# Kernel tuning notes

Measured on AMD Instinct MI355X. Metric: run time of the kernel, lower is better.

## Reference

```python
import jax, jax.numpy as jnp
import numpy as np

TEMPERATURE = 8.0  # sqrt(d_k=64)

def setup_inputs() -> dict:
    key = jax.random.key(0)
    kq, kk, kv = jax.random.split(key, 3)
    B, S, D = 32, 2048, 64  # B = batch*heads
    q = jax.random.normal(kq, (B, S, D), dtype=jnp.float32)
    k = jax.random.normal(kk, (B, S, D), dtype=jnp.float32)
    v = jax.random.normal(kv, (B, S, D), dtype=jnp.float32)
    return {"q": q, "k": k, "v": v}

def reference(q, k, v):
    # attn = softmax((q @ k^T) / temperature) along key dim; dropout = identity (eval)
    attn = jnp.einsum('bqd,bkd->bqk', q, k) / TEMPERATURE  # [B, S, S]
    attn = jax.nn.softmax(attn, axis=2)
    out = jnp.einsum('bqk,bkd->bqd', attn, v)              # [B, S, D]
    return out
```

## Files before the change

### kernel.cpp

```cpp
#include <hip/hip_runtime.h>
#include <stdint.h>


#define BATCH 32
#define SEQ   2048
#define DIM   64
#define QBLK_WAVE 32
#define NWAVES 4
#define QBLK  (QBLK_WAVE*NWAVES)
#define KVBLK 64
#define NT    (SEQ/KVBLK)

typedef __attribute__((ext_vector_type(8)))  __bf16   bf16x8;
typedef __attribute__((ext_vector_type(16))) float    f32x16;
typedef __attribute__((ext_vector_type(2)))  unsigned uint2v;
typedef __attribute__((ext_vector_type(4)))  unsigned uint4v;

static __device__ __forceinline__ unsigned cvt_pk(float lo, float hi) {
    unsigned r; asm("v_cvt_pk_bf16_f32 %0, %1, %2" : "=v"(r) : "v"(lo), "v"(hi)); return r;
}
static __device__ __forceinline__ float exp2v(float x) {
    float r; asm("v_exp_f32 %0, %1" : "=v"(r) : "v"(x)); return r;
}
static __device__ __forceinline__ float other_half(float v, int hi) {
    unsigned u = __builtin_bit_cast(unsigned, v);
    uint2v r = __builtin_amdgcn_permlane32_swap(u, u, false, false);
    return __builtin_bit_cast(float, hi ? r[0] : r[1]);
}

#define MFMA32(A, B, C) __builtin_amdgcn_mfma_f32_32x32x16_bf16((A), (B), (C), 0, 0, 0)
#define TRR(dst, OFFSTR) \
    asm volatile("ds_read_b64_tr_b16 %0, %1 offset:" OFFSTR : "=v"(dst) : "v"(trbase))

static __device__ __forceinline__ bf16x8 frag_of(uint2v r0, uint2v r1) {
    uint4v w = { r0[0], r0[1], r1[0], r1[1] };
    return __builtin_bit_cast(bf16x8, w);
}

__global__ __launch_bounds__(256, 2)
void attn_fwd_kernel(const float* __restrict__ q,
                     const float* __restrict__ k,
                     const float* __restrict__ v,
                     float* __restrict__ out)
{
    __shared__ unsigned short Ksh[KVBLK * DIM];
    __shared__ unsigned short Vsh[KVBLK * DIM];

    const int id    = blockIdx.x;
    const int swz   = (id & 7) * ((SEQ / QBLK) * BATCH / 8) + (id >> 3);
    const int batch = swz >> 4;
    const int qtile = swz & 15;

    const int t    = threadIdx.x;
    const int lane = t & 63;
    const int wid  = t >> 6;
    const int hi   = lane >> 5;
    const int l31  = lane & 31;
    const int l7   = lane & 7;

    const size_t bbase = (size_t)batch * SEQ * DIM;
    const int q0w = qtile * QBLK + wid * QBLK_WAVE;

    bf16x8 qf[4];
    {
        const float sc = 0.125f * 1.44269504088896341f;
        const float* qp = q + bbase + (size_t)(q0w + l31) * DIM + hi * 8;
        #pragma unroll
        for (int dblk = 0; dblk < 4; ++dblk) {
            float4 f0 = *(const float4*)(qp + dblk * 16);
            float4 f1 = *(const float4*)(qp + dblk * 16 + 4);
            uint4v w = { cvt_pk(f0.x * sc, f0.y * sc), cvt_pk(f0.z * sc, f0.w * sc),
                         cvt_pk(f1.x * sc, f1.y * sc), cvt_pk(f1.z * sc, f1.w * sc) };
            qf[dblk] = __builtin_bit_cast(bf16x8, w);
        }
    }

    const int srow = t >> 2, sq = t & 3;
    const float* kg = k + bbase + (size_t)srow * DIM + sq * 16;
    const float* vg = v + bbase + (size_t)srow * DIM + sq * 16;
    const int ch0 = ((2 * sq)     ^ (srow & 7)) * 8;
    const int ch1 = ((2 * sq + 1) ^ (srow & 7)) * 8;
    unsigned short* ksta = &Ksh[srow * DIM];
    unsigned short* vsta = &Vsh[srow * DIM];

    const int bq = (l31 & 15) >> 2, ee = (lane >> 4) & 1, cc = lane & 3;
    const unsigned vb = (unsigned)(uintptr_t)Vsh;
    const unsigned trbase = vb + (unsigned)((8 * hi + bq) * 128 +
                                            (((2 * ee + (cc >> 1)) ^ bq) * 16) + (cc & 1) * 8);

    const unsigned short* krow = &Ksh[l31 * DIM];

    f32x16 oacc0, oacc1;
    #pragma unroll
    for (int r = 0; r < 16; ++r) { oacc0[r] = 0.f; oacc1[r] = 0.f; }
    float m_run = -3.0e38f, l_run = 0.0f;

    float4 rk[4], rv[4];
    #pragma unroll
    for (int i = 0; i < 4; ++i) {
        rk[i] = *(const float4*)(kg + i * 4);
        rv[i] = *(const float4*)(vg + i * 4);
    }

    #pragma unroll 1
    for (int tile = 0; tile < NT; ++tile) {
        __syncthreads();

        {
            uint4v kw0 = { cvt_pk(rk[0].x, rk[0].y), cvt_pk(rk[0].z, rk[0].w),
                           cvt_pk(rk[1].x, rk[1].y), cvt_pk(rk[1].z, rk[1].w) };
            uint4v kw1 = { cvt_pk(rk[2].x, rk[2].y), cvt_pk(rk[2].z, rk[2].w),
                           cvt_pk(rk[3].x, rk[3].y), cvt_pk(rk[3].z, rk[3].w) };
            uint4v vw0 = { cvt_pk(rv[0].x, rv[0].y), cvt_pk(rv[0].z, rv[0].w),
                           cvt_pk(rv[1].x, rv[1].y), cvt_pk(rv[1].z, rv[1].w) };
            uint4v vw1 = { cvt_pk(rv[2].x, rv[2].y), cvt_pk(rv[2].z, rv[2].w),
                           cvt_pk(rv[3].x, rv[3].y), cvt_pk(rv[3].z, rv[3].w) };
            *(uint4v*)&ksta[ch0] = kw0;
            *(uint4v*)&ksta[ch1] = kw1;
            *(uint4v*)&vsta[ch0] = vw0;
            *(uint4v*)&vsta[ch1] = vw1;
        }
        if (tile + 1 < NT) {
            const float* kg2 = kg + (size_t)(tile + 1) * KVBLK * DIM;
            const float* vg2 = vg + (size_t)(tile + 1) * KVBLK * DIM;
            #pragma unroll
            for (int i = 0; i < 4; ++i) {
                rk[i] = *(const float4*)(kg2 + i * 4);
                rv[i] = *(const float4*)(vg2 + i * 4);
            }
        }
        __syncthreads();

        f32x16 s0, s1;
        #pragma unroll
        for (int r = 0; r < 16; ++r) { s0[r] = 0.f; s1[r] = 0.f; }
        #pragma unroll
        for (int dblk = 0; dblk < 4; ++dblk) {
            int cofs = (((2 * dblk + hi) ^ l7) * 8);
            bf16x8 kf0 = *(const bf16x8*)&krow[cofs];
            bf16x8 kf1 = *(const bf16x8*)&krow[32 * DIM + cofs];
            s0 = MFMA32(kf0, qf[dblk], s0);
            s1 = MFMA32(kf1, qf[dblk], s1);
        }

        uint2v m0k0r0, m0k0r1, m0k1r0, m0k1r1, m0k2r0, m0k2r1, m0k3r0, m0k3r1;
        uint2v m1k0r0, m1k0r1, m1k1r0, m1k1r1, m1k2r0, m1k2r1, m1k3r0, m1k3r1;
        TRR(m0k0r0, "0");    TRR(m0k0r1, "576");
        TRR(m0k1r0, "2048"); TRR(m0k1r1, "2624");
        TRR(m0k2r0, "4096"); TRR(m0k2r1, "4672");
        TRR(m0k3r0, "6144"); TRR(m0k3r1, "6720");
        TRR(m1k0r0, "64");   TRR(m1k0r1, "512");
        TRR(m1k1r0, "2112"); TRR(m1k1r1, "2560");
        TRR(m1k2r0, "4160"); TRR(m1k2r1, "4608");
        TRR(m1k3r0, "6208"); TRR(m1k3r1, "6656");

        float tm = s0[0];
        #pragma unroll
        for (int r = 1; r < 16; ++r) tm = fmaxf(tm, s0[r]);
        #pragma unroll
        for (int r = 0; r < 16; ++r) tm = fmaxf(tm, s1[r]);
        tm = fmaxf(tm, other_half(tm, hi));
        float mn    = fmaxf(m_run, tm);
        float alpha = exp2v(m_run - mn);
        m_run = mn;
        float rs = 0.f;
        #pragma unroll
        for (int r = 0; r < 16; ++r) { s0[r] = exp2v(s0[r] - mn); rs += s0[r]; }
        #pragma unroll
        for (int r = 0; r < 16; ++r) { s1[r] = exp2v(s1[r] - mn); rs += s1[r]; }
        rs += other_half(rs, hi);
        l_run = l_run * alpha + rs;
        #pragma unroll
        for (int r = 0; r < 16; ++r) { oacc0[r] *= alpha; oacc1[r] *= alpha; }

        bf16x8 bfr0, bfr1, bfr2, bfr3;
        {
            uint2v x1 = __builtin_amdgcn_permlane32_swap(cvt_pk(s0[0], s0[1]),  cvt_pk(s0[4], s0[5]),  false, false);
            uint2v x2 = __builtin_amdgcn_permlane32_swap(cvt_pk(s0[2], s0[3]),  cvt_pk(s0[6], s0[7]),  false, false);
            uint4v w = { x1[0], x2[0], x1[1], x2[1] };
            bfr0 = __builtin_bit_cast(bf16x8, w);
            uint2v y1 = __builtin_amdgcn_permlane32_swap(cvt_pk(s0[8], s0[9]),  cvt_pk(s0[12], s0[13]), false, false);
            uint2v y2 = __builtin_amdgcn_permlane32_swap(cvt_pk(s0[10], s0[11]), cvt_pk(s0[14], s0[15]), false, false);
            uint4v w2 = { y1[0], y2[0], y1[1], y2[1] };
            bfr1 = __builtin_bit_cast(bf16x8, w2);
            uint2v z1 = __builtin_amdgcn_permlane32_swap(cvt_pk(s1[0], s1[1]),  cvt_pk(s1[4], s1[5]),  false, false);
            uint2v z2 = __builtin_amdgcn_permlane32_swap(cvt_pk(s1[2], s1[3]),  cvt_pk(s1[6], s1[7]),  false, false);
            uint4v w3 = { z1[0], z2[0], z1[1], z2[1] };
            bfr2 = __builtin_bit_cast(bf16x8, w3);
            uint2v u1 = __builtin_amdgcn_permlane32_swap(cvt_pk(s1[8], s1[9]),  cvt_pk(s1[12], s1[13]), false, false);
            uint2v u2 = __builtin_amdgcn_permlane32_swap(cvt_pk(s1[10], s1[11]), cvt_pk(s1[14], s1[15]), false, false);
            uint4v w4 = { u1[0], u2[0], u1[1], u2[1] };
            bfr3 = __builtin_bit_cast(bf16x8, w4);
        }

        asm volatile("s_waitcnt lgkmcnt(0)" ::: "memory");
        __builtin_amdgcn_sched_barrier(0);

        oacc0 = MFMA32(frag_of(m0k0r0, m0k0r1), bfr0, oacc0);
        oacc1 = MFMA32(frag_of(m1k0r0, m1k0r1), bfr0, oacc1);
        oacc0 = MFMA32(frag_of(m0k1r0, m0k1r1), bfr1, oacc0);
        oacc1 = MFMA32(frag_of(m1k1r0, m1k1r1), bfr1, oacc1);
        oacc0 = MFMA32(frag_of(m0k2r0, m0k2r1), bfr2, oacc0);
        oacc1 = MFMA32(frag_of(m1k2r0, m1k2r1), bfr2, oacc1);
        oacc0 = MFMA32(frag_of(m0k3r0, m0k3r1), bfr3, oacc0);
        oacc1 = MFMA32(frag_of(m1k3r0, m1k3r1), bfr3, oacc1);
    }

    float invl = 1.0f / l_run;
    float* op = out + bbase + (size_t)(q0w + l31) * DIM + 4 * hi;
    #pragma unroll
    for (int rq = 0; rq < 4; ++rq) {
        float4 o0 = { oacc0[4 * rq] * invl, oacc0[4 * rq + 1] * invl,
                      oacc0[4 * rq + 2] * invl, oacc0[4 * rq + 3] * invl };
        float4 o1 = { oacc1[4 * rq] * invl, oacc1[4 * rq + 1] * invl,
                      oacc1[4 * rq + 2] * invl, oacc1[4 * rq + 3] * invl };
        *(float4*)(op + 8 * rq)      = o0;
        *(float4*)(op + 32 + 8 * rq) = o1;
    }
}

extern "C" void kernel_launch(void* const* d_in, const int* in_sizes, int n_in,
                              void* d_out, int out_size, void* d_ws, size_t ws_size,
                              hipStream_t stream) {
    const float* q = (const float*)d_in[0];
    const float* k = (const float*)d_in[1];
    const float* v = (const float*)d_in[2];
    float* out = (float*)d_out;
    dim3 grid((SEQ / QBLK) * BATCH);
    dim3 block(256);
    hipLaunchKernelGGL(attn_fwd_kernel, grid, block, 0, stream, q, k, v, out);
}
```

Measured before the change: 137.5 us.

## Double-buffer K/V in LDS, lazy softmax rescale, tree reductions, MFMA priority

Splits K/V shared memory into two buffers so the next tile is converted and stored while the current one is consumed, leaving one barrier per iteration instead of two. The online softmax now rescales the accumulators only when the row max rises by more than a threshold, skipping most exp and multiply work. Max and sum reductions become trees for more ILP, and s_setprio raises priority around MFMA blocks. The tradeoff is twice the LDS footprint, which may limit occupancy, plus less numerical headroom from the deferred rescaling.

```diff
diff --git a/kernel.cpp b/kernel.cpp
--- a/kernel.cpp
+++ b/kernel.cpp
@@ -10,6 +10,7 @@
 #define QBLK  (QBLK_WAVE*NWAVES)
 #define KVBLK 64
 #define NT    (SEQ/KVBLK)
+#define BUFSHORTS (KVBLK*DIM)
 
 typedef __attribute__((ext_vector_type(8)))  __bf16   bf16x8;
 typedef __attribute__((ext_vector_type(16))) float    f32x16;
@@ -30,7 +31,9 @@
 
 #define MFMA32(A, B, C) __builtin_amdgcn_mfma_f32_32x32x16_bf16((A), (B), (C), 0, 0, 0)
 #define TRR(dst, OFFSTR) \
-    asm volatile("ds_read_b64_tr_b16 %0, %1 offset:" OFFSTR : "=v"(dst) : "v"(trbase))
+    asm volatile("ds_read_b64_tr_b16 %0, %1 offset:" OFFSTR : "=v"(dst) : "v"(trb))
+#define MAX4(a,b,c,d) fmaxf(fmaxf((a),(b)), fmaxf((c),(d)))
+#define SUM4(a,b,c,d) (((a)+(b)) + ((c)+(d)))
 
 static __device__ __forceinline__ bf16x8 frag_of(uint2v r0, uint2v r1) {
     uint4v w = { r0[0], r0[1], r1[0], r1[1] };
@@ -43,8 +46,8 @@
                      const float* __restrict__ v,
                      float* __restrict__ out)
 {
-    __shared__ unsigned short Ksh[KVBLK * DIM];
-    __shared__ unsigned short Vsh[KVBLK * DIM];
+    __shared__ unsigned short Ksh[2][BUFSHORTS];
+    __shared__ unsigned short Vsh[2][BUFSHORTS];
 
     const int id    = blockIdx.x;
     const int swz   = (id & 7) * ((SEQ / QBLK) * BATCH / 8) + (id >> 3);
@@ -80,20 +83,16 @@
     const float* vg = v + bbase + (size_t)srow * DIM + sq * 16;
     const int ch0 = ((2 * sq)     ^ (srow & 7)) * 8;
     const int ch1 = ((2 * sq + 1) ^ (srow & 7)) * 8;
-    unsigned short* ksta = &Ksh[srow * DIM];
-    unsigned short* vsta = &Vsh[srow * DIM];
 
     const int bq = (l31 & 15) >> 2, ee = (lane >> 4) & 1, cc = lane & 3;
-    const unsigned vb = (unsigned)(uintptr_t)Vsh;
+    const unsigned vb = (unsigned)(uintptr_t)&Vsh[0][0];
     const unsigned trbase = vb + (unsigned)((8 * hi + bq) * 128 +
                                             (((2 * ee + (cc >> 1)) ^ bq) * 16) + (cc & 1) * 8);
 
-    const unsigned short* krow = &Ksh[l31 * DIM];
-
     f32x16 oacc0, oacc1;
     #pragma unroll
     for (int r = 0; r < 16; ++r) { oacc0[r] = 0.f; oacc1[r] = 0.f; }
-    float m_run = -3.0e38f, l_run = 0.0f;
+    float m_run = 0.0f, l_run = 0.0f;
 
     float4 rk[4], rv[4];
     #pragma unroll
@@ -101,39 +100,40 @@
         rk[i] = *(const float4*)(kg + i * 4);
         rv[i] = *(const float4*)(vg + i * 4);
     }
-
-    #pragma unroll 1
+    {
+        uint4v kw0 = { cvt_pk(rk[0].x, rk[0].y), cvt_pk(rk[0].z, rk[0].w),
+                       cvt_pk(rk[1].x, rk[1].y), cvt_pk(rk[1].z, rk[1].w) };
+        uint4v kw1 = { cvt_pk(rk[2].x, rk[2].y), cvt_pk(rk[2].z, rk[2].w),
+                       cvt_pk(rk[3].x, rk[3].y), cvt_pk(rk[3].z, rk[3].w) };
+        uint4v vw0 = { cvt_pk(rv[0].x, rv[0].y), cvt_pk(rv[0].z, rv[0].w),
+                       cvt_pk(rv[1].x, rv[1].y), cvt_pk(rv[1].z, rv[1].w) };
+        uint4v vw1 = { cvt_pk(rv[2].x, rv[2].y), cvt_pk(rv[2].z, rv[2].w),
+                       cvt_pk(rv[3].x, rv[3].y), cvt_pk(rv[3].z, rv[3].w) };
+        *(uint4v*)&Ksh[0][srow * DIM + ch0] = kw0;
+        *(uint4v*)&Ksh[0][srow * DIM + ch1] = kw1;
+        *(uint4v*)&Vsh[0][srow * DIM + ch0] = vw0;
+        *(uint4v*)&Vsh[0][srow * DIM + ch1] = vw1;
+    }
+    #pragma unroll
+    for (int i = 0; i < 4; ++i) {
+        rk[i] = *(const float4*)(kg + KVBLK * DIM + i * 4);
+        rv[i] = *(const float4*)(vg + KVBLK * DIM + i * 4);
+    }
+    asm volatile("s_waitcnt lgkmcnt(0)" ::: "memory");
+
+    #pragma unroll 2
     for (int tile = 0; tile < NT; ++tile) {
-        __syncthreads();
-
-        {
-            uint4v kw0 = { cvt_pk(rk[0].x, rk[0].y), cvt_pk(rk[0].z, rk[0].w),
-                           cvt_pk(rk[1].x, rk[1].y), cvt_pk(rk[1].z, rk[1].w) };
-            uint4v kw1 = { cvt_pk(rk[2].x, rk[2].y), cvt_pk(rk[2].z, rk[2].w),
-                           cvt_pk(rk[3].x, rk[3].y), cvt_pk(rk[3].z, rk[3].w) };
-            uint4v vw0 = { cvt_pk(rv[0].x, rv[0].y), cvt_pk(rv[0].z, rv[0].w),
-                           cvt_pk(rv[1].x, rv[1].y), cvt_pk(rv[1].z, rv[1].w) };
-            uint4v vw1 = { cvt_pk(rv[2].x, rv[2].y), cvt_pk(rv[2].z, rv[2].w),
-                           cvt_pk(rv[3].x, rv[3].y), cvt_pk(rv[3].z, rv[3].w) };
-            *(uint4v*)&ksta[ch0] = kw0;
-            *(uint4v*)&ksta[ch1] = kw1;
-            *(uint4v*)&vsta[ch0] = vw0;
-            *(uint4v*)&vsta[ch1] = vw1;
-        }
-        if (tile + 1 < NT) {
-            const float* kg2 = kg + (size_t)(tile + 1) * KVBLK * DIM;
-            const float* vg2 = vg + (size_t)(tile + 1) * KVBLK * DIM;
-            #pragma unroll
-            for (int i = 0; i < 4; ++i) {
-                rk[i] = *(const float4*)(kg2 + i * 4);
-                rv[i] = *(const float4*)(vg2 + i * 4);
-            }
-        }
-        __syncthreads();
+        const int cur = tile & 1;
+        __builtin_amdgcn_s_barrier();
+        __builtin_amdgcn_sched_barrier(0);
+
+        const unsigned short* krow = &Ksh[cur][l31 * DIM];
+        const unsigned trb = trbase + (unsigned)(cur * (2 * BUFSHORTS));
 
         f32x16 s0, s1;
         #pragma unroll
         for (int r = 0; r < 16; ++r) { s0[r] = 0.f; s1[r] = 0.f; }
+        __builtin_amdgcn_s_setprio(1);
         #pragma unroll
         for (int dblk = 0; dblk < 4; ++dblk) {
             int cofs = (((2 * dblk + hi) ^ l7) * 8);
@@ -142,6 +142,7 @@
             s0 = MFMA32(kf0, qf[dblk], s0);
             s1 = MFMA32(kf1, qf[dblk], s1);
         }
+        __builtin_amdgcn_s_setprio(0);
 
         uint2v m0k0r0, m0k0r1, m0k1r0, m0k1r1, m0k2r0, m0k2r1, m0k3r0, m0k3r1;
         uint2v m1k0r0, m1k0r1, m1k1r0, m1k1r1, m1k2r0, m1k2r1, m1k3r0, m1k3r1;
@@ -154,31 +155,51 @@
         TRR(m1k2r0, "4160"); TRR(m1k2r1, "4608");
         TRR(m1k3r0, "6208"); TRR(m1k3r1, "6656");
 
-        float tm = s0[0];
-        #pragma unroll
-        for (int r = 1; r < 16; ++r) tm = fmaxf(tm, s0[r]);
-        #pragma unroll
-        for (int r = 0; r < 16; ++r) tm = fmaxf(tm, s1[r]);
-        tm = fmaxf(tm, other_half(tm, hi));
-        float mn    = fmaxf(m_run, tm);
-        float alpha = exp2v(m_run - mn);
-        m_run = mn;
-        float rs = 0.f;
-        #pragma unroll
-        for (int r = 0; r < 16; ++r) { s0[r] = exp2v(s0[r] - mn); rs += s0[r]; }
-        #pragma unroll
-        for (int r = 0; r < 16; ++r) { s1[r] = exp2v(s1[r] - mn); rs += s1[r]; }
-        rs += other_half(rs, hi);
-        l_run = l_run * alpha + rs;
-        #pragma unroll
-        for (int r = 0; r < 16; ++r) { oacc0[r] *= alpha; oacc1[r] *= alpha; }
+        {
+            float a0 = MAX4(s0[0], s0[1], s0[2],  s0[3]);
+            float a1 = MAX4(s0[4], s0[5], s0[6],  s0[7]);
+            float a2 = MAX4(s0[8], s0[9], s0[10], s0[11]);
+            float a3 = MAX4(s0[12], s0[13], s0[14], s0[15]);
+            float b0 = MAX4(s1[0], s1[1], s1[2],  s1[3]);
+            float b1 = MAX4(s1[4], s1[5], s1[6],  s1[7]);
+            float b2 = MAX4(s1[8], s1[9], s1[10], s1[11]);
+            float b3 = MAX4(s1[12], s1[13], s1[14], s1[15]);
+            float pmax = MAX4(MAX4(a0, a1, a2, a3), b0, b1, b2);
+            pmax = fmaxf(pmax, b3);
+            pmax = fmaxf(pmax, other_half(pmax, hi));
+            if (!__all(pmax - m_run <= 12.0f)) {
+                float mn    = fmaxf(m_run, pmax);
+                float alpha = exp2v(m_run - mn);
+                m_run = mn;
+                l_run *= alpha;
+                #pragma unroll
+                for (int r = 0; r < 16; ++r) { oacc0[r] *= alpha; oacc1[r] *= alpha; }
+            }
+        }
+        #pragma unroll
+        for (int r = 0; r < 16; ++r) s0[r] = exp2v(s0[r] - m_run);
+        #pragma unroll
+        for (int r = 0; r < 16; ++r) s1[r] = exp2v(s1[r] - m_run);
+        {
+            float a0 = SUM4(s0[0], s0[1], s0[2],  s0[3]);
+            float a1 = SUM4(s0[4], s0[5], s0[6],  s0[7]);
+            float a2 = SUM4(s0[8], s0[9], s0[10], s0[11]);
+            float a3 = SUM4(s0[12], s0[13], s0[14], s0[15]);
+            float b0 = SUM4(s1[0], s1[1], s1[2],  s1[3]);
+            float b1 = SUM4(s1[4], s1[5], s1[6],  s1[7]);
+            float b2 = SUM4(s1[8], s1[9], s1[10], s1[11]);
+            float b3 = SUM4(s1[12], s1[13], s1[14], s1[15]);
+            float rs = SUM4(SUM4(a0, a1, a2, a3), b0, b1, b2) + b3;
+            rs += other_half(rs, hi);
+            l_run += rs;
+        }
 
         bf16x8 bfr0, bfr1, bfr2, bfr3;
         {
             uint2v x1 = __builtin_amdgcn_permlane32_swap(cvt_pk(s0[0], s0[1]),  cvt_pk(s0[4], s0[5]),  false, false);
             uint2v x2 = __builtin_amdgcn_permlane32_swap(cvt_pk(s0[2], s0[3]),  cvt_pk(s0[6], s0[7]),  false, false);
-            uint4v w = { x1[0], x2[0], x1[1], x2[1] };
-            bfr0 = __builtin_bit_cast(bf16x8, w);
+            uint4v w1 = { x1[0], x2[0], x1[1], x2[1] };
+            bfr0 = __builtin_bit_cast(bf16x8, w1);
             uint2v y1 = __builtin_amdgcn_permlane32_swap(cvt_pk(s0[8], s0[9]),  cvt_pk(s0[12], s0[13]), false, false);
             uint2v y2 = __builtin_amdgcn_permlane32_swap(cvt_pk(s0[10], s0[11]), cvt_pk(s0[14], s0[15]), false, false);
             uint4v w2 = { y1[0], y2[0], y1[1], y2[1] };
@@ -193,9 +214,36 @@
             bfr3 = __builtin_bit_cast(bf16x8, w4);
         }
 
+        if (tile + 1 < NT) {
+            unsigned short* kst = &Ksh[cur ^ 1][srow * DIM];
+            unsigned short* vst = &Vsh[cur ^ 1][srow * DIM];
+            uint4v kw0 = { cvt_pk(rk[0].x, rk[0].y), cvt_pk(rk[0].z, rk[0].w),
+                           cvt_pk(rk[1].x, rk[1].y), cvt_pk(rk[1].z, rk[1].w) };
+            uint4v kw1 = { cvt_pk(rk[2].x, rk[2].y), cvt_pk(rk[2].z, rk[2].w),
+                           cvt_pk(rk[3].x, rk[3].y), cvt_pk(rk[3].z, rk[3].w) };
+            uint4v vw0 = { cvt_pk(rv[0].x, rv[0].y), cvt_pk(rv[0].z, rv[0].w),
+                           cvt_pk(rv[1].x, rv[1].y), cvt_pk(rv[1].z, rv[1].w) };
+            uint4v vw1 = { cvt_pk(rv[2].x, rv[2].y), cvt_pk(rv[2].z, rv[2].w),
+                           cvt_pk(rv[3].x, rv[3].y), cvt_pk(rv[3].z, rv[3].w) };
+            *(uint4v*)&kst[ch0] = kw0;
+            *(uint4v*)&kst[ch1] = kw1;
+            *(uint4v*)&vst[ch0] = vw0;
+            *(uint4v*)&vst[ch1] = vw1;
+        }
+        if (tile + 2 < NT) {
+            const float* kp = kg + (size_t)(tile + 2) * KVBLK * DIM;
+            const float* vp = vg + (size_t)(tile + 2) * KVBLK * DIM;
+            #pragma unroll
+            for (int i = 0; i < 4; ++i) {
+                rk[i] = *(const float4*)(kp + i * 4);
+                rv[i] = *(const float4*)(vp + i * 4);
+            }
+        }
+
         asm volatile("s_waitcnt lgkmcnt(0)" ::: "memory");
         __builtin_amdgcn_sched_barrier(0);
 
+        __builtin_amdgcn_s_setprio(1);
         oacc0 = MFMA32(frag_of(m0k0r0, m0k0r1), bfr0, oacc0);
         oacc1 = MFMA32(frag_of(m1k0r0, m1k0r1), bfr0, oacc1);
         oacc0 = MFMA32(frag_of(m0k1r0, m0k1r1), bfr1, oacc0);
@@ -204,6 +252,7 @@
         oacc1 = MFMA32(frag_of(m1k2r0, m1k2r1), bfr2, oacc1);
         oacc0 = MFMA32(frag_of(m0k3r0, m0k3r1), bfr3, oacc0);
         oacc1 = MFMA32(frag_of(m1k3r0, m1k3r1), bfr3, oacc1);
+        __builtin_amdgcn_s_setprio(0);
     }
 
     float invl = 1.0f / l_run;
```

After: 133.2 us. 1.03x faster.
